# Optimization experiments

Hardware: AMD Instinct MI355X
Metric: run time of the kernel (lower is better)

## Reference

```python
import jax, jax.numpy as jnp
import numpy as np

C = 256
DK = C // 8  # query/key channels


def setup_inputs() -> dict:
    key = jax.random.key(0)
    ks = jax.random.split(key, 7)
    B, W, H = 4, 64, 64
    x = jax.random.normal(ks[0], (B, C, W, H), dtype=jnp.float32)
    s_in = 1.0 / np.sqrt(C)
    Wq = jax.random.normal(ks[1], (DK, C), dtype=jnp.float32) * s_in
    bq = jnp.zeros((DK,), dtype=jnp.float32)
    Wk = jax.random.normal(ks[2], (DK, C), dtype=jnp.float32) * s_in
    bk = jnp.zeros((DK,), dtype=jnp.float32)
    Wv = jax.random.normal(ks[3], (C, C), dtype=jnp.float32) * s_in
    bv = jnp.zeros((C,), dtype=jnp.float32)
    return {"x": x, "Wq": Wq, "bq": bq, "Wk": Wk, "bk": bk, "Wv": Wv, "bv": bv}


def reference(x, Wq, bq, Wk, bk, Wv, bv):
    B, Cc, W, H = x.shape
    N = W * H
    xf = x.reshape(B, Cc, N)  # (B, C, N) flattened spatial
    # 1x1 convs == channel matmuls
    q = jnp.einsum('dc,bcn->bnd', Wq, xf) + bq  # (B, N, DK)
    k = jnp.einsum('dc,bcn->bdn', Wk, xf) + bk[None, :, None]  # (B, DK, N)
    v = jnp.einsum('oc,bcn->bon', Wv, xf) + bv[None, :, None]  # (B, C, N)
    energy = jnp.einsum('bnd,bdm->bnm', q, k) / jnp.sqrt(jnp.float32(q.shape[-1]))
    attn = jax.nn.softmax(energy, axis=-1)  # (B, N, N)
    out = jnp.einsum('bcn,bmn->bcm', v, attn)  # v @ attn^T
    return out.reshape(B, Cc, W, H) + x
```

## Files before the change

### kernel.cpp

```cpp
#include <hip/hip_runtime.h>
#include <hip/hip_bf16.h>
#include <math.h>

#define BB 4
#define CC 256
#define DKK 32
#define NN 4096
#define QSCALE2 0.25503489022324213f

typedef __attribute__((ext_vector_type(8))) __bf16 bf16x8;
typedef __attribute__((ext_vector_type(4))) __bf16 bf16x4;
typedef __attribute__((ext_vector_type(4))) float f32x4;
typedef __attribute__((ext_vector_type(16))) float f32x16;

#define XROW 264

__global__ __launch_bounds__(256) void qkv2_kernel(
    const float* __restrict__ x,
    const float* __restrict__ Wq, const float* __restrict__ Wk,
    const float* __restrict__ Wv,
    const float* __restrict__ bq, const float* __restrict__ bk,
    const float* __restrict__ bv,
    __bf16* __restrict__ qws, __bf16* __restrict__ kws, __bf16* __restrict__ vws)
{
    __shared__ __align__(16) unsigned char smemB[32 * XROW * 2];
    __bf16* xs = (__bf16*)smemB;
    float (*scr)[33] = (float (*)[33])smemB;

    const int tid = threadIdx.x;
    const int w   = tid >> 6;
    const int l   = tid & 63;
    const int l15 = l & 15;
    const int lq  = l >> 4;
    const int n0  = blockIdx.x * 32;
    const int b   = blockIdx.y;

    {
        const int cl = tid >> 3;
        const int nf = (tid & 7) * 4;
#pragma unroll
        for (int p = 0; p < 8; p++) {
            int c = p * 32 + cl;
            float4 v = *(const float4*)&x[((size_t)(b * CC + c)) * NN + n0 + nf];
            xs[(nf + 0) * XROW + c] = (__bf16)v.x;
            xs[(nf + 1) * XROW + c] = (__bf16)v.y;
            xs[(nf + 2) * XROW + c] = (__bf16)v.z;
            xs[(nf + 3) * XROW + c] = (__bf16)v.w;
        }
    }

    const float* wrow[5];
#pragma unroll
    for (int ot = 0; ot < 5; ot++) {
        int ob = 80 * w + ot * 16;
        const float* mat; int r0;
        if (ob < 32)      { mat = Wq; r0 = ob; }
        else if (ob < 64) { mat = Wk; r0 = ob - 32; }
        else              { mat = Wv; r0 = ob - 64; }
        wrow[ot] = mat + (size_t)(r0 + l15) * CC + lq * 8;
    }

    __syncthreads();

    const f32x4 zf = {0.f, 0.f, 0.f, 0.f};
    f32x4 acc[5][2];
#pragma unroll
    for (int i = 0; i < 5; i++)
#pragma unroll
        for (int j = 0; j < 2; j++) acc[i][j] = zf;

    const __bf16* xls = &xs[l15 * XROW + lq * 8];

    bf16x8 bcur[2], acur[5], bnxt[2], anxt[5];
#pragma unroll
    for (int nt = 0; nt < 2; nt++) bcur[nt] = *(const bf16x8*)(xls + nt * 16 * XROW);
#pragma unroll
    for (int ot = 0; ot < 5; ot++) {
        f32x4 a0 = *(const f32x4*)(wrow[ot]);
        f32x4 a1 = *(const f32x4*)(wrow[ot] + 4);
        bf16x8 af;
#pragma unroll
        for (int j = 0; j < 4; j++) { af[j] = (__bf16)a0[j]; af[4 + j] = (__bf16)a1[j]; }
        acur[ot] = af;
    }

#pragma unroll
    for (int ks = 0; ks < 8; ks++) {
        if (ks < 7) {
#pragma unroll
            for (int nt = 0; nt < 2; nt++)
                bnxt[nt] = *(const bf16x8*)(xls + nt * 16 * XROW + (ks + 1) * 32);
#pragma unroll
            for (int ot = 0; ot < 5; ot++) {
                f32x4 a0 = *(const f32x4*)(wrow[ot] + (ks + 1) * 32);
                f32x4 a1 = *(const f32x4*)(wrow[ot] + (ks + 1) * 32 + 4);
                bf16x8 af;
#pragma unroll
                for (int j = 0; j < 4; j++) { af[j] = (__bf16)a0[j]; af[4 + j] = (__bf16)a1[j]; }
                anxt[ot] = af;
            }
        }
#pragma unroll
        for (int ot = 0; ot < 5; ot++)
#pragma unroll
            for (int nt = 0; nt < 2; nt++)
                acc[ot][nt] = __builtin_amdgcn_mfma_f32_16x16x32_bf16(acur[ot], bcur[nt], acc[ot][nt], 0, 0, 0);
        if (ks < 7) {
#pragma unroll
            for (int nt = 0; nt < 2; nt++) bcur[nt] = bnxt[nt];
#pragma unroll
            for (int ot = 0; ot < 5; ot++) acur[ot] = anxt[ot];
        }
    }

    __syncthreads();

    __bf16* vchunk = vws + (size_t)b * CC * NN + (size_t)(n0 >> 5) * 8192;
#pragma unroll
    for (int ot = 0; ot < 5; ot++) {
        int ob = 80 * w + ot * 16;
#pragma unroll
        for (int nt = 0; nt < 2; nt++) {
#pragma unroll
            for (int r = 0; r < 4; r++) {
                int o = ob + lq * 4 + r;
                int n = nt * 16 + l15;
                float val = acc[ot][nt][r];
                if (ob >= 64) {
                    int c  = o - 64;
                    int ct = c >> 5, c5 = c & 31;
                    vchunk[ct * 1024 + nt * 512 + c5 * 16 + l15] =
                        (__bf16)(val + bv[c]);
                } else if (ob < 32) {
                    scr[o][n] = (val + bq[o]) * QSCALE2;
                } else {
                    scr[o][n] = val + bk[o - 32];
                }
            }
        }
    }
    __syncthreads();
    {
        int n  = tid >> 3;
        int d0 = (tid & 7) * 4;
        bf16x4 qv, kv;
#pragma unroll
        for (int j = 0; j < 4; j++) {
            qv[j] = (__bf16)scr[d0 + j][n];
            kv[j] = (__bf16)scr[32 + d0 + j][n];
        }
        size_t base = ((size_t)b * NN + n0 + n) * DKK + d0;
        *(bf16x4*)&qws[base] = qv;
        *(bf16x4*)&kws[base] = kv;
    }
}

#define MST 68

__global__ __launch_bounds__(256, 2) void attn_kernel(
    const __bf16* __restrict__ qb, const __bf16* __restrict__ kb,
    const __bf16* __restrict__ vt, const float* __restrict__ x,
    float* __restrict__ out)
{
    __shared__ __align__(16) unsigned char smem[36096];
    const int tid = threadIdx.x;
    const int w   = tid >> 6;
    const int l   = tid & 63;
    const int m31 = l & 31;
    const int hi  = l >> 5;
    float* Ls   = (float*)(smem + 34816);
    float* Linv = (float*)(smem + 35840);

    const int beta = blockIdx.x;
    const int b    = (beta >> 1) & 3;
    const int ch   = (beta >> 3) & 1;
    const int mt64 = ((beta >> 4) << 1) | (beta & 1);
    const int m0   = mt64 * 64;

    const __bf16* qbb = qb + (size_t)b * NN * DKK;
    const __bf16* kbb = kb + (size_t)b * NN * DKK;
    const __bf16* vtb = vt + (size_t)b * CC * NN;

    bf16x8 qa[2][2];
#pragma unroll
    for (int mt = 0; mt < 2; mt++)
#pragma unroll
        for (int kk = 0; kk < 2; kk++)
            qa[mt][kk] = *(const bf16x8*)(qbb + (size_t)(m0 + mt * 32 + m31) * DKK + kk * 16 + hi * 8);

    const __bf16* kstrip = kbb + (size_t)(w * 32 + m31) * DKK + hi * 8;
    const __bf16* vstrip = vtb + (size_t)w * 8192 + (size_t)ch * 4096
                               + m31 * 16 + hi * 8;

    const f32x16 zf16 = {0.f,0.f,0.f,0.f,0.f,0.f,0.f,0.f,
                         0.f,0.f,0.f,0.f,0.f,0.f,0.f,0.f};
    f32x16 acc[4][2];
#pragma unroll
    for (int ct = 0; ct < 4; ct++)
#pragma unroll
        for (int mt = 0; mt < 2; mt++) acc[ct][mt] = zf16;
    float lacc[2] = {0.f, 0.f};

    union PU { unsigned u[4]; bf16x8 v; };
    auto kq_pack = [&](bf16x8 kA0, bf16x8 kA1, bf16x8 (&pf)[2][2]) {
#pragma unroll
        for (int mt = 0; mt < 2; mt++) {
            f32x16 e = __builtin_amdgcn_mfma_f32_32x32x16_bf16(kA0, qa[mt][0], zf16, 0, 0, 0);
            e = __builtin_amdgcn_mfma_f32_32x32x16_bf16(kA1, qa[mt][1], e, 0, 0, 0);
            float s = 0.f;
            unsigned g[4][2];
#pragma unroll
            for (int gi = 0; gi < 4; gi++) {
                bf16x4 pb;
#pragma unroll
                for (int t = 0; t < 4; t++) {
                    float v = __builtin_amdgcn_exp2f(e[4 * gi + t]);
                    s += v; pb[t] = (__bf16)v;
                }
                PU tu; *(bf16x4*)tu.u = pb;
                g[gi][0] = tu.u[0]; g[gi][1] = tu.u[1];
            }
            lacc[mt] += s;
#pragma unroll
            for (int kk = 0; kk < 2; kk++) {
                PU r;
#pragma unroll
                for (int wi = 0; wi < 2; wi++) {
                    auto sw = __builtin_amdgcn_permlane32_swap(
                        (int)g[kk * 2][wi], (int)g[kk * 2 + 1][wi], false, false);
                    r.u[wi]     = (unsigned)sw[0];
                    r.u[2 + wi] = (unsigned)sw[1];
                }
                pf[mt][kk] = r.v;
            }
        }
    };

    bf16x8 kA0 = *(const bf16x8*)kstrip;
    bf16x8 kA1 = *(const bf16x8*)(kstrip + 16);
#pragma unroll 2
    for (int ic = 0; ic < 32; ic++) {
        const __bf16* vch = vstrip + (size_t)ic * 32768;

        bf16x8 vA[4];
#pragma unroll
        for (int ct = 0; ct < 4; ct++)
            vA[ct] = *(const bf16x8*)(vch + ct * 1024);

        bf16x8 pf[2][2];
        kq_pack(kA0, kA1, pf);

        kA0 = *(const bf16x8*)(kstrip + (size_t)(ic + 1) * 128 * DKK);
        kA1 = *(const bf16x8*)(kstrip + (size_t)(ic + 1) * 128 * DKK + 16);

        bf16x8 vB[4];
#pragma unroll
        for (int ct = 0; ct < 4; ct++)
            vB[ct] = *(const bf16x8*)(vch + ct * 1024 + 512);

        __builtin_amdgcn_s_setprio(1);
#pragma unroll
        for (int ct = 0; ct < 4; ct++)
#pragma unroll
            for (int mt = 0; mt < 2; mt++) {
                acc[ct][mt] = __builtin_amdgcn_mfma_f32_32x32x16_bf16(vA[ct], pf[mt][0], acc[ct][mt], 0, 0, 0);
                acc[ct][mt] = __builtin_amdgcn_mfma_f32_32x32x16_bf16(vB[ct], pf[mt][1], acc[ct][mt], 0, 0, 0);
            }
        __builtin_amdgcn_s_setprio(0);
    }

#pragma unroll
    for (int mt = 0; mt < 2; mt++) lacc[mt] += __shfl_xor(lacc[mt], 32, 64);
    if (hi == 0) {
#pragma unroll
        for (int mt = 0; mt < 2; mt++) Ls[w * 64 + mt * 32 + m31] = lacc[mt];
    }
    __syncthreads();
    if (tid < 64)
        Linv[tid] = 1.0f / (Ls[tid] + Ls[64 + tid] + Ls[128 + tid] + Ls[192 + tid]);

    float* Ored = (float*)smem + w * (32 * MST);
#pragma unroll
    for (int q = 0; q < 4; q++) {
        if (q > 0) __syncthreads();
#pragma unroll
        for (int mt = 0; mt < 2; mt++)
#pragma unroll
            for (int reg = 0; reg < 16; reg++) {
                int crow = (reg & 3) + 8 * (reg >> 2) + 4 * hi;
                Ored[crow * MST + mt * 32 + m31] = acc[q][mt][reg];
            }
        __syncthreads();
        const int cl  = tid >> 3;
        const int mi0 = (tid & 7) * 8;
        const float* Ob = (const float*)smem + cl * MST;
#pragma unroll
        for (int j = 0; j < 2; j++) {
            int mi = mi0 + 4 * j;
            f32x4 s = *(const f32x4*)&Ob[mi];
            s = s + *(const f32x4*)&Ob[1 * (32 * MST) + mi];
            s = s + *(const f32x4*)&Ob[2 * (32 * MST) + mi];
            s = s + *(const f32x4*)&Ob[3 * (32 * MST) + mi];
            f32x4 li = *(const f32x4*)&Linv[mi];
            int c = ch * 128 + q * 32 + cl;
            size_t gi = ((size_t)(b * CC + c)) * NN + m0 + mi;
            f32x4 xr = *(const f32x4*)&x[gi];
            *(f32x4*)&out[gi] = s * li + xr;
        }
    }
}

extern "C" void kernel_launch(void* const* d_in, const int* in_sizes, int n_in,
                              void* d_out, int out_size, void* d_ws, size_t ws_size,
                              hipStream_t stream) {
    const float* x  = (const float*)d_in[0];
    const float* Wq = (const float*)d_in[1];
    const float* bq = (const float*)d_in[2];
    const float* Wk = (const float*)d_in[3];
    const float* bk = (const float*)d_in[4];
    const float* Wv = (const float*)d_in[5];
    const float* bv = (const float*)d_in[6];
    float* out = (float*)d_out;

    __bf16* qws = (__bf16*)d_ws;
    __bf16* kws = qws + (size_t)BB * NN * DKK;
    __bf16* vws = kws + (size_t)BB * NN * DKK;

    qkv2_kernel<<<dim3(128, BB), 256, 0, stream>>>(x, Wq, Wk, Wv, bq, bk, bv,
                                                   qws, kws, vws);
    attn_kernel<<<dim3(512), 256, 0, stream>>>(qws, kws, vws, x, out);
}
```

Baseline: 156.0 us.

## Software-pipeline QK softmax packing one chunk ahead of PV MFMAs

```diff
diff --git a/kernel.cpp b/kernel.cpp
--- a/kernel.cpp
+++ b/kernel.cpp
@@ -236,28 +236,11 @@
         }
     };
 
-    bf16x8 kA0 = *(const bf16x8*)kstrip;
-    bf16x8 kA1 = *(const bf16x8*)(kstrip + 16);
-#pragma unroll 2
-    for (int ic = 0; ic < 32; ic++) {
-        const __bf16* vch = vstrip + (size_t)ic * 32768;
-
-        bf16x8 vA[4];
-#pragma unroll
-        for (int ct = 0; ct < 4; ct++)
-            vA[ct] = *(const bf16x8*)(vch + ct * 1024);
-
-        bf16x8 pf[2][2];
-        kq_pack(kA0, kA1, pf);
-
-        kA0 = *(const bf16x8*)(kstrip + (size_t)(ic + 1) * 128 * DKK);
-        kA1 = *(const bf16x8*)(kstrip + (size_t)(ic + 1) * 128 * DKK + 16);
-
+    auto pv_step = [&](const __bf16* vch, bf16x8 (&pf)[2][2], bf16x8 (&vA)[4]) {
         bf16x8 vB[4];
 #pragma unroll
         for (int ct = 0; ct < 4; ct++)
             vB[ct] = *(const bf16x8*)(vch + ct * 1024 + 512);
-
         __builtin_amdgcn_s_setprio(1);
 #pragma unroll
         for (int ct = 0; ct < 4; ct++)
@@ -267,6 +250,42 @@
                 acc[ct][mt] = __builtin_amdgcn_mfma_f32_32x32x16_bf16(vB[ct], pf[mt][1], acc[ct][mt], 0, 0, 0);
             }
         __builtin_amdgcn_s_setprio(0);
+    };
+
+    bf16x8 pfA[2][2], pfB[2][2];
+    bf16x8 kA0 = *(const bf16x8*)kstrip;
+    bf16x8 kA1 = *(const bf16x8*)(kstrip + 16);
+    kq_pack(kA0, kA1, pfA);
+    kA0 = *(const bf16x8*)(kstrip + (size_t)128 * DKK);
+    kA1 = *(const bf16x8*)(kstrip + (size_t)128 * DKK + 16);
+
+#pragma unroll 1
+    for (int icp = 0; icp < 16; icp++) {
+        const int ic0 = icp * 2;
+        {
+            const __bf16* vch = vstrip + (size_t)ic0 * 32768;
+            bf16x8 vA[4];
+#pragma unroll
+            for (int ct = 0; ct < 4; ct++)
+                vA[ct] = *(const bf16x8*)(vch + ct * 1024);
+            kq_pack(kA0, kA1, pfB);
+            kA0 = *(const bf16x8*)(kstrip + (size_t)(ic0 + 2) * 128 * DKK);
+            kA1 = *(const bf16x8*)(kstrip + (size_t)(ic0 + 2) * 128 * DKK + 16);
+            pv_step(vch, pfA, vA);
+        }
+        {
+            const __bf16* vch = vstrip + (size_t)(ic0 + 1) * 32768;
+            bf16x8 vA[4];
+#pragma unroll
+            for (int ct = 0; ct < 4; ct++)
+                vA[ct] = *(const bf16x8*)(vch + ct * 1024);
+            if (icp < 15) {
+                kq_pack(kA0, kA1, pfA);
+                kA0 = *(const bf16x8*)(kstrip + (size_t)(ic0 + 3) * 128 * DKK);
+                kA1 = *(const bf16x8*)(kstrip + (size_t)(ic0 + 3) * 128 * DKK + 16);
+            }
+            pv_step(vch, pfB, vA);
+        }
     }
 
 #pragma unroll
```

Result: faster. 151.5 us (-2.9%).

## Split attention work by channel per wave and share probabilities via LDS

Applied to the files above, without the earlier changes.

```diff
diff --git a/kernel.cpp b/kernel.cpp
--- a/kernel.cpp
+++ b/kernel.cpp
@@ -155,158 +155,133 @@
     }
 }
 
-#define MST 68
-
-__global__ __launch_bounds__(256, 2) void attn_kernel(
+__global__ __launch_bounds__(256, 4) void attn_kernel(
     const __bf16* __restrict__ qb, const __bf16* __restrict__ kb,
     const __bf16* __restrict__ vt, const float* __restrict__ x,
     float* __restrict__ out)
 {
-    __shared__ __align__(16) unsigned char smem[36096];
+    __shared__ __align__(16) unsigned char smem[17536];
+    unsigned char* pbuf = smem;
+    float* Ls   = (float*)(smem + 16384);
+    float* Linv = (float*)(smem + 17408);
+
     const int tid = threadIdx.x;
     const int w   = tid >> 6;
     const int l   = tid & 63;
     const int m31 = l & 31;
     const int hi  = l >> 5;
-    float* Ls   = (float*)(smem + 34816);
-    float* Linv = (float*)(smem + 35840);
 
     const int beta = blockIdx.x;
     const int b    = (beta >> 1) & 3;
     const int ch   = (beta >> 3) & 1;
-    const int mt64 = ((beta >> 4) << 1) | (beta & 1);
-    const int m0   = mt64 * 64;
+    const int mt32 = ((beta >> 4) << 1) | (beta & 1);
+    const int m0   = mt32 * 32;
 
     const __bf16* qbb = qb + (size_t)b * NN * DKK;
     const __bf16* kbb = kb + (size_t)b * NN * DKK;
     const __bf16* vtb = vt + (size_t)b * CC * NN;
 
-    bf16x8 qa[2][2];
-#pragma unroll
-    for (int mt = 0; mt < 2; mt++)
-#pragma unroll
-        for (int kk = 0; kk < 2; kk++)
-            qa[mt][kk] = *(const bf16x8*)(qbb + (size_t)(m0 + mt * 32 + m31) * DKK + kk * 16 + hi * 8);
+    bf16x8 qa[2];
+#pragma unroll
+    for (int kk = 0; kk < 2; kk++)
+        qa[kk] = *(const bf16x8*)(qbb + (size_t)(m0 + m31) * DKK + kk * 16 + hi * 8);
 
     const __bf16* kstrip = kbb + (size_t)(w * 32 + m31) * DKK + hi * 8;
-    const __bf16* vstrip = vtb + (size_t)w * 8192 + (size_t)ch * 4096
-                               + m31 * 16 + hi * 8;
+    const __bf16* vstrip = vtb + (size_t)(ch * 4 + w) * 1024 + m31 * 16 + hi * 8;
 
     const f32x16 zf16 = {0.f,0.f,0.f,0.f,0.f,0.f,0.f,0.f,
                          0.f,0.f,0.f,0.f,0.f,0.f,0.f,0.f};
-    f32x16 acc[4][2];
-#pragma unroll
-    for (int ct = 0; ct < 4; ct++)
-#pragma unroll
-        for (int mt = 0; mt < 2; mt++) acc[ct][mt] = zf16;
-    float lacc[2] = {0.f, 0.f};
+    f32x16 acc = zf16;
+    float lacc = 0.f;
 
     union PU { unsigned u[4]; bf16x8 v; };
-    auto kq_pack = [&](bf16x8 kA0, bf16x8 kA1, bf16x8 (&pf)[2][2]) {
-#pragma unroll
-        for (int mt = 0; mt < 2; mt++) {
-            f32x16 e = __builtin_amdgcn_mfma_f32_32x32x16_bf16(kA0, qa[mt][0], zf16, 0, 0, 0);
-            e = __builtin_amdgcn_mfma_f32_32x32x16_bf16(kA1, qa[mt][1], e, 0, 0, 0);
-            float s = 0.f;
-            unsigned g[4][2];
-#pragma unroll
-            for (int gi = 0; gi < 4; gi++) {
-                bf16x4 pb;
-#pragma unroll
-                for (int t = 0; t < 4; t++) {
-                    float v = __builtin_amdgcn_exp2f(e[4 * gi + t]);
-                    s += v; pb[t] = (__bf16)v;
-                }
-                PU tu; *(bf16x4*)tu.u = pb;
-                g[gi][0] = tu.u[0]; g[gi][1] = tu.u[1];
-            }
-            lacc[mt] += s;
+    auto kq_store = [&](int buf, bf16x8 k0, bf16x8 k1) {
+        f32x16 e = __builtin_amdgcn_mfma_f32_32x32x16_bf16(k0, qa[0], zf16, 0, 0, 0);
+        e = __builtin_amdgcn_mfma_f32_32x32x16_bf16(k1, qa[1], e, 0, 0, 0);
+        float s = 0.f;
+        unsigned g[4][2];
+#pragma unroll
+        for (int gi = 0; gi < 4; gi++) {
+            bf16x4 pb;
+#pragma unroll
+            for (int t = 0; t < 4; t++) {
+                float v = __builtin_amdgcn_exp2f(e[4 * gi + t]);
+                s += v; pb[t] = (__bf16)v;
+            }
+            PU tu; *(bf16x4*)tu.u = pb;
+            g[gi][0] = tu.u[0]; g[gi][1] = tu.u[1];
+        }
+        lacc += s;
+#pragma unroll
+        for (int kk = 0; kk < 2; kk++) {
+            PU r;
+#pragma unroll
+            for (int wi = 0; wi < 2; wi++) {
+                auto sw = __builtin_amdgcn_permlane32_swap(
+                    (int)g[kk * 2][wi], (int)g[kk * 2 + 1][wi], false, false);
+                r.u[wi]     = (unsigned)sw[0];
+                r.u[2 + wi] = (unsigned)sw[1];
+            }
+            *(bf16x8*)(pbuf + buf * 8192 + w * 2048 + kk * 1024 + hi * 512 + m31 * 16) = r.v;
+        }
+    };
+
+    {
+        bf16x8 k0 = *(const bf16x8*)kstrip;
+        bf16x8 k1 = *(const bf16x8*)(kstrip + 16);
+        kq_store(0, k0, k1);
+    }
+    bf16x8 kA0 = *(const bf16x8*)(kstrip + (size_t)128 * DKK);
+    bf16x8 kA1 = *(const bf16x8*)(kstrip + (size_t)128 * DKK + 16);
+    __syncthreads();
+
+#pragma unroll 1
+    for (int ic = 0; ic < 32; ic++) {
+        const int cur = ic & 1;
+        const __bf16* vch = vstrip + (size_t)ic * 32768;
+
+        bf16x8 vf[8];
+#pragma unroll
+        for (int j = 0; j < 4; j++)
+#pragma unroll
+            for (int kk = 0; kk < 2; kk++)
+                vf[j * 2 + kk] = *(const bf16x8*)(vch + j * 8192 + kk * 512);
+
+        if (ic < 31) {
+            kq_store(cur ^ 1, kA0, kA1);
+            kA0 = *(const bf16x8*)(kstrip + (size_t)(ic + 2) * 128 * DKK);
+            kA1 = *(const bf16x8*)(kstrip + (size_t)(ic + 2) * 128 * DKK + 16);
+        }
+
+        __builtin_amdgcn_s_setprio(1);
+#pragma unroll
+        for (int j = 0; j < 4; j++)
 #pragma unroll
             for (int kk = 0; kk < 2; kk++) {
-                PU r;
-#pragma unroll
-                for (int wi = 0; wi < 2; wi++) {
-                    auto sw = __builtin_amdgcn_permlane32_swap(
-                        (int)g[kk * 2][wi], (int)g[kk * 2 + 1][wi], false, false);
-                    r.u[wi]     = (unsigned)sw[0];
-                    r.u[2 + wi] = (unsigned)sw[1];
-                }
-                pf[mt][kk] = r.v;
-            }
-        }
-    };
-
-    bf16x8 kA0 = *(const bf16x8*)kstrip;
-    bf16x8 kA1 = *(const bf16x8*)(kstrip + 16);
-#pragma unroll 2
-    for (int ic = 0; ic < 32; ic++) {
-        const __bf16* vch = vstrip + (size_t)ic * 32768;
-
-        bf16x8 vA[4];
-#pragma unroll
-        for (int ct = 0; ct < 4; ct++)
-            vA[ct] = *(const bf16x8*)(vch + ct * 1024);
-
-        bf16x8 pf[2][2];
-        kq_pack(kA0, kA1, pf);
-
-        kA0 = *(const bf16x8*)(kstrip + (size_t)(ic + 1) * 128 * DKK);
-        kA1 = *(const bf16x8*)(kstrip + (size_t)(ic + 1) * 128 * DKK + 16);
-
-        bf16x8 vB[4];
-#pragma unroll
-        for (int ct = 0; ct < 4; ct++)
-            vB[ct] = *(const bf16x8*)(vch + ct * 1024 + 512);
-
-        __builtin_amdgcn_s_setprio(1);
-#pragma unroll
-        for (int ct = 0; ct < 4; ct++)
-#pragma unroll
-            for (int mt = 0; mt < 2; mt++) {
-                acc[ct][mt] = __builtin_amdgcn_mfma_f32_32x32x16_bf16(vA[ct], pf[mt][0], acc[ct][mt], 0, 0, 0);
-                acc[ct][mt] = __builtin_amdgcn_mfma_f32_32x32x16_bf16(vB[ct], pf[mt][1], acc[ct][mt], 0, 0, 0);
+                bf16x8 pf = *(const bf16x8*)(pbuf + cur * 8192 + j * 2048 + kk * 1024 + hi * 512 + m31 * 16);
+                acc = __builtin_amdgcn_mfma_f32_32x32x16_bf16(vf[j * 2 + kk], pf, acc, 0, 0, 0);
             }
         __builtin_amdgcn_s_setprio(0);
-    }
-
-#pragma unroll
-    for (int mt = 0; mt < 2; mt++) lacc[mt] += __shfl_xor(lacc[mt], 32, 64);
-    if (hi == 0) {
-#pragma unroll
-        for (int mt = 0; mt < 2; mt++) Ls[w * 64 + mt * 32 + m31] = lacc[mt];
-    }
-    __syncthreads();
-    if (tid < 64)
-        Linv[tid] = 1.0f / (Ls[tid] + Ls[64 + tid] + Ls[128 + tid] + Ls[192 + tid]);
-
-    float* Ored = (float*)smem + w * (32 * MST);
-#pragma unroll
-    for (int q = 0; q < 4; q++) {
-        if (q > 0) __syncthreads();
-#pragma unroll
-        for (int mt = 0; mt < 2; mt++)
-#pragma unroll
-            for (int reg = 0; reg < 16; reg++) {
-                int crow = (reg & 3) + 8 * (reg >> 2) + 4 * hi;
-                Ored[crow * MST + mt * 32 + m31] = acc[q][mt][reg];
-            }
         __syncthreads();
-        const int cl  = tid >> 3;
-        const int mi0 = (tid & 7) * 8;
-        const float* Ob = (const float*)smem + cl * MST;
-#pragma unroll
-        for (int j = 0; j < 2; j++) {
-            int mi = mi0 + 4 * j;
-            f32x4 s = *(const f32x4*)&Ob[mi];
-            s = s + *(const f32x4*)&Ob[1 * (32 * MST) + mi];
-            s = s + *(const f32x4*)&Ob[2 * (32 * MST) + mi];
-            s = s + *(const f32x4*)&Ob[3 * (32 * MST) + mi];
-            f32x4 li = *(const f32x4*)&Linv[mi];
-            int c = ch * 128 + q * 32 + cl;
-            size_t gi = ((size_t)(b * CC + c)) * NN + m0 + mi;
-            f32x4 xr = *(const f32x4*)&x[gi];
-            *(f32x4*)&out[gi] = s * li + xr;
-        }
+    }
+
+    Ls[(w * 2 + hi) * 32 + m31] = lacc;
+    __syncthreads();
+    if (tid < 32) {
+        float s = 0.f;
+#pragma unroll
+        for (int r = 0; r < 8; r++) s += Ls[r * 32 + tid];
+        Linv[tid] = 1.0f / s;
+    }
+    __syncthreads();
+    const float li = Linv[m31];
+
+#pragma unroll
+    for (int reg = 0; reg < 16; reg++) {
+        int crow = (reg & 3) + 8 * (reg >> 2) + 4 * hi;
+        int c = ch * 128 + w * 32 + crow;
+        size_t gi = ((size_t)(b * CC + c)) * NN + m0 + m31;
+        out[gi] = acc[reg] * li + x[gi];
     }
 }
 
@@ -328,5 +303,5 @@
 
     qkv2_kernel<<<dim3(128, BB), 256, 0, stream>>>(x, Wq, Wk, Wv, bq, bk, bv,
                                                    qws, kws, vws);
-    attn_kernel<<<dim3(512), 256, 0, stream>>>(qws, kws, vws, x, out);
+    attn_kernel<<<dim3(1024), 256, 0, stream>>>(qws, kws, vws, x, out);
 }
```

Measured after the change: 163.2 us. 1.05x slower.
